# Optimization experiments

Hardware: AMD Instinct MI355X
Metric: run time of the kernel (lower is better)

Reference implementation:

```python
import jax, jax.numpy as jnp
import numpy as np

H = 4096        # hidden_size
NH = 32         # num query heads
NKV = 8         # num kv heads
D = H // NH     # head_dim = 128
S = 2048        # num tokens (single causal sequence)
THETA = 1000000.0
SCALE = D ** -0.5


def _rope(x, positions):
    # neox-style (rotate-half) RoPE over full head_dim, as vLLM's get_rope default
    half = D // 2
    inv_freq = 1.0 / (THETA ** (jnp.arange(half, dtype=jnp.float32) / half))
    ang = positions.astype(jnp.float32)[:, None] * inv_freq          # [S, D/2]
    cos = jnp.cos(ang)[:, None, :]                                   # [S, 1, D/2]
    sin = jnp.sin(ang)[:, None, :]
    x1, x2 = x[..., :half], x[..., half:]
    return jnp.concatenate([x1 * cos - x2 * sin, x2 * cos + x1 * sin], axis=-1)


def setup_inputs() -> dict:
    key = jax.random.key(0)
    k1, k2, k3 = jax.random.split(key, 3)
    positions = jnp.arange(S, dtype=jnp.int32)
    hidden_states = jax.random.normal(k1, (S, H), dtype=jnp.float32)
    w_qkv = jax.random.normal(k2, ((NH + 2 * NKV) * D, H), dtype=jnp.float32) * 0.02
    w_o = jax.random.normal(k3, (H, NH * D), dtype=jnp.float32) * 0.02
    return {"positions": positions, "hidden_states": hidden_states,
            "w_qkv": w_qkv, "w_o": w_o}


def reference(positions, hidden_states, w_qkv, w_o):
    # fused QKV projection (Linear, bias=False): x @ W^T
    qkv = hidden_states @ w_qkv.T                                    # [S, (NH+2*NKV)*D]
    q, k, v = jnp.split(qkv, [NH * D, (NH + NKV) * D], axis=-1)
    q = q.reshape(S, NH, D)
    k = k.reshape(S, NKV, D)
    v = v.reshape(S, NKV, D)
    # RoPE on q and k
    q = _rope(q, positions)
    k = _rope(k, positions)
    # GQA causal attention: group NH query heads onto NKV kv heads
    g = NH // NKV
    qg = q.reshape(S, NKV, g, D)
    scores = jnp.einsum('qhgd,khd->hgqk', qg, k) * SCALE             # [NKV, g, S, S]
    causal = positions[:, None] >= positions[None, :]                # [S, S]
    scores = jnp.where(causal[None, None], scores, jnp.float32(-1e30))
    probs = jax.nn.softmax(scores, axis=-1)
    o = jnp.einsum('hgqk,khd->qhgd', probs, v).reshape(S, NH * D)
    return o @ w_o.T                                                 # [S, H]
```

## Files before the change

### kernel.cpp

```cpp
#include <hip/hip_runtime.h>
#include <hip/hip_bf16.h>

#define S_LEN 2048
#define HID 4096
#define NH 32
#define NKV 8
#define DH 128
#define QKV_N ((NH + 2 * NKV) * DH)
#define SCALE_ATT 0.08838834764831845f
#define SCALE2_ATT 0.12751744f

typedef __bf16 bf16;
typedef __bf16 bf16x8 __attribute__((ext_vector_type(8)));
typedef __bf16 bf16x4 __attribute__((ext_vector_type(4)));
typedef float f32x4 __attribute__((ext_vector_type(4)));
typedef float f32x16 __attribute__((ext_vector_type(16)));

__device__ inline f32x4 mfma16(bf16x8 a, bf16x8 b, f32x4 c) {
    return __builtin_amdgcn_mfma_f32_16x16x32_bf16(a, b, c, 0, 0, 0);
}
__device__ inline f32x16 mfma32(bf16x8 a, bf16x8 b, f32x16 c) {
    return __builtin_amdgcn_mfma_f32_32x32x16_bf16(a, b, c, 0, 0, 0);
}

__device__ inline bf16x8 load8(const float* p) {
    const float4 a = ((const float4*)p)[0];
    const float4 b = ((const float4*)p)[1];
    bf16x8 r;
    r[0] = (bf16)a.x; r[1] = (bf16)a.y; r[2] = (bf16)a.z; r[3] = (bf16)a.w;
    r[4] = (bf16)b.x; r[5] = (bf16)b.y; r[6] = (bf16)b.z; r[7] = (bf16)b.w;
    return r;
}
__device__ inline bf16x8 load8(const bf16* p) { return *(const bf16x8*)p; }

__device__ inline void load_lds16(const bf16* g, bf16* lds_base) {
    __builtin_amdgcn_global_load_lds(
        (const __attribute__((address_space(1))) void*)g,
        (__attribute__((address_space(3))) void*)lds_base, 16, 0, 0);
}

__device__ inline unsigned pack2_bf16(float lo, float hi) {
    union { bf16 h[2]; unsigned u; } r;
    r.h[0] = (bf16)lo;
    r.h[1] = (bf16)hi;
    return r.u;
}

__global__ __launch_bounds__(256) void cvt3_kernel(const float* __restrict__ s0, bf16* __restrict__ d0, int c0,
                                                   const float* __restrict__ s1, bf16* __restrict__ d1, int c1,
                                                   const float* __restrict__ s2, bf16* __restrict__ d2, int c2) {
    int i = blockIdx.x * 256 + threadIdx.x;
    if (i < c0) { *(bf16x8*)&d0[(size_t)i * 8] = load8(&s0[(size_t)i * 8]); return; }
    i -= c0;
    if (i < c1) { *(bf16x8*)&d1[(size_t)i * 8] = load8(&s1[(size_t)i * 8]); return; }
    i -= c1;
    if (i < c2) { *(bf16x8*)&d2[(size_t)i * 8] = load8(&s2[(size_t)i * 8]); }
}

template <int BN, typename OutT>
__global__ __launch_bounds__(512, 2) void gemm_8ph(const bf16* __restrict__ A,
                                                   const bf16* __restrict__ B,
                                                   OutT* __restrict__ C,
                                                   int K, int lda, int ldc) {
    constexpr int WTN = BN / 4;
    constexpr int NREP = WTN / 32;
    constexpr int BLOADS = BN / 64;
    extern __shared__ char smem[];
    bf16* As = (bf16*)smem;
    bf16* Bs = (bf16*)(smem + 2 * 256 * 64 * 2);

    const int tid = threadIdx.x;
    const int lane = tid & 63;
    const int w = tid >> 6;
    const int wm = w >> 2;
    const int wn = w & 3;
    const int ln = lane & 31;
    const int hi = lane >> 5;
    const int rseg = lane >> 3;
    const int gc = (lane & 7) ^ rseg;

    const int m0 = (int)blockIdx.y * 256;
    const int n0 = (int)blockIdx.x * BN;

    const int NT = K >> 6;

    auto stage = [&](int b, int kt) {
        const int k0 = kt * 64;
        const bf16* Ag = &A[(size_t)(m0 + w * 32 + rseg) * lda + k0 + gc * 8];
        bf16* Al = &As[b * (256 * 64) + (w * 32) * 64];
#pragma unroll
        for (int j = 0; j < 4; ++j)
            load_lds16(Ag + (size_t)j * 8 * lda, Al + j * 512);
        const bf16* Bg = &B[(size_t)(n0 + w * (BN / 8) + rseg) * K + k0 + gc * 8];
        bf16* Bl = &Bs[b * (BN * 64) + (w * (BN / 8)) * 64];
#pragma unroll
        for (int j = 0; j < BLOADS; ++j)
            load_lds16(Bg + (size_t)j * 8 * K, Bl + j * 512);
    };

    f32x16 acc[4][NREP];
#pragma unroll
    for (int mi = 0; mi < 4; ++mi)
#pragma unroll
        for (int j = 0; j < NREP; ++j)
#pragma unroll
            for (int r = 0; r < 16; ++r) acc[mi][j][r] = 0.f;

    stage(0, 0);
    int buf = 0;
    for (int kt = 0; kt < NT; ++kt) {
        if (kt + 1 < NT) {
            stage(buf ^ 1, kt + 1);
            if constexpr (BN == 256)
                asm volatile("s_waitcnt vmcnt(8)" ::: "memory");
            else
                asm volatile("s_waitcnt vmcnt(6)" ::: "memory");
        } else {
            asm volatile("s_waitcnt vmcnt(0)" ::: "memory");
        }
        __builtin_amdgcn_s_barrier();
        __builtin_amdgcn_sched_barrier(0);

        const bf16* Ab = &As[buf * (256 * 64)];
        const bf16* Bb = &Bs[buf * (BN * 64)];
        bf16x8 bfr[NREP][4];
#pragma unroll
        for (int j = 0; j < NREP; ++j)
#pragma unroll
            for (int kk = 0; kk < 4; ++kk) {
                const int n = wn * WTN + j * 32 + ln;
                bfr[j][kk] = *(const bf16x8*)&Bb[n * 64 + (((2 * kk + hi) ^ (ln & 7)) * 8)];
            }
#pragma unroll
        for (int p = 0; p < 2; ++p) {
            bf16x8 af[2][4];
#pragma unroll
            for (int i = 0; i < 2; ++i)
#pragma unroll
                for (int kk = 0; kk < 4; ++kk) {
                    const int m = wm * 128 + (p * 2 + i) * 32 + ln;
                    af[i][kk] = *(const bf16x8*)&Ab[m * 64 + (((2 * kk + hi) ^ (ln & 7)) * 8)];
                }
            __builtin_amdgcn_s_setprio(1);
#pragma unroll
            for (int i = 0; i < 2; ++i)
#pragma unroll
                for (int j = 0; j < NREP; ++j)
#pragma unroll
                    for (int kk = 0; kk < 4; ++kk)
                        acc[p * 2 + i][j] = mfma32(af[i][kk], bfr[j][kk], acc[p * 2 + i][j]);
            __builtin_amdgcn_s_setprio(0);
        }
        __builtin_amdgcn_sched_barrier(0);
        asm volatile("s_waitcnt lgkmcnt(0)" ::: "memory");
        __builtin_amdgcn_s_barrier();
        __builtin_amdgcn_sched_barrier(0);
        buf ^= 1;
    }

#pragma unroll
    for (int mi = 0; mi < 4; ++mi)
#pragma unroll
        for (int j = 0; j < NREP; ++j)
#pragma unroll
            for (int r = 0; r < 16; ++r) {
                int row = m0 + wm * 128 + mi * 32 + (r & 3) + 8 * (r >> 2) + 4 * hi;
                int col = n0 + wn * WTN + j * 32 + ln;
                C[(size_t)row * ldc + col] = (OutT)acc[mi][j][r];
            }
}

template <typename AT, typename OutT>
__global__ __launch_bounds__(256) void gemm_bt(const AT* __restrict__ A,
                                               const float* __restrict__ B,
                                               OutT* __restrict__ C,
                                               int K, int lda, int ldc) {
    const int tid = threadIdx.x;
    const int lane = tid & 63;
    const int w = tid >> 6;
    const int m0 = blockIdx.y * 128;
    const int n0 = blockIdx.x * 128;
    const int wm = (w >> 1) * 64;
    const int wn = (w & 1) * 64;
    const int ln = lane & 15;
    const int qo = lane >> 4;

    __shared__ bf16 As[128 * 72];
    __shared__ bf16 Bs[128 * 72];

    f32x4 acc[4][4];
#pragma unroll
    for (int mi = 0; mi < 4; ++mi)
#pragma unroll
        for (int ni = 0; ni < 4; ++ni) acc[mi][ni] = f32x4{0.f, 0.f, 0.f, 0.f};

    for (int k0 = 0; k0 < K; k0 += 64) {
#pragma unroll
        for (int i = 0; i < 4; ++i) {
            int v = tid + i * 256;
            int row = v >> 3;
            int col = (v & 7) * 8;
            *(bf16x8*)&As[row * 72 + col] = load8(&A[(size_t)(m0 + row) * lda + k0 + col]);
            *(bf16x8*)&Bs[row * 72 + col] = load8(&B[(size_t)(n0 + row) * K + k0 + col]);
        }
        __syncthreads();
#pragma unroll
        for (int kk = 0; kk < 64; kk += 32) {
            bf16x8 af[4], bfr[4];
#pragma unroll
            for (int mi = 0; mi < 4; ++mi)
                af[mi] = *(const bf16x8*)&As[(wm + mi * 16 + ln) * 72 + kk + qo * 8];
#pragma unroll
            for (int ni = 0; ni < 4; ++ni)
                bfr[ni] = *(const bf16x8*)&Bs[(wn + ni * 16 + ln) * 72 + kk + qo * 8];
#pragma unroll
            for (int mi = 0; mi < 4; ++mi)
#pragma unroll
                for (int ni = 0; ni < 4; ++ni)
                    acc[mi][ni] = mfma16(af[mi], bfr[ni], acc[mi][ni]);
        }
        __syncthreads();
    }
#pragma unroll
    for (int mi = 0; mi < 4; ++mi)
#pragma unroll
        for (int ni = 0; ni < 4; ++ni)
#pragma unroll
            for (int r = 0; r < 4; ++r) {
                int row = m0 + wm + mi * 16 + qo * 4 + r;
                int col = n0 + wn + ni * 16 + ln;
                C[(size_t)row * ldc + col] = (OutT)acc[mi][ni][r];
            }
}

__global__ __launch_bounds__(256) void rope_kernel(bf16* __restrict__ qkv,
                                                   const int* __restrict__ positions) {
    int idx = blockIdx.x * 256 + threadIdx.x;
    const int total = S_LEN * (NH + NKV) * 64;
    if (idx >= total) return;
    int d = idx & 63;
    int t = idx >> 6;
    int head = t % (NH + NKV);
    int s = t / (NH + NKV);
    size_t base = (size_t)s * QKV_N + (head < NH ? head * DH : NH * DH + (head - NH) * DH);
    float x1 = (float)qkv[base + d];
    float x2 = (float)qkv[base + d + 64];
    float pos = (float)positions[s];
    float inv = expf(-0.21586735246819178f * (float)d);
    float ang = pos * inv;
    float c = cosf(ang);
    float sn = sinf(ang);
    qkv[base + d] = (bf16)(x1 * c - x2 * sn);
    qkv[base + d + 64] = (bf16)(x2 * c + x1 * sn);
}

__global__ __launch_bounds__(256) void vtrans_kernel(const bf16* __restrict__ qkv,
                                                     bf16* __restrict__ vt_g) {
    const int tid = threadIdx.x;
    const int s0 = blockIdx.x * 64;
    const int kvh = blockIdx.y;
    __shared__ bf16 Ls[64 * 136];
#pragma unroll
    for (int i = 0; i < 4; ++i) {
        int v = tid + i * 256;
        int row = v >> 4;
        int col = (v & 15) * 8;
        *(bf16x8*)&Ls[row * 136 + col] =
            *(const bf16x8*)&qkv[(size_t)(s0 + row) * QKV_N + (NH + NKV) * DH + kvh * DH + col];
    }
    __syncthreads();
#pragma unroll
    for (int i = 0; i < 4; ++i) {
        int u = tid + i * 256;
        int d = u >> 3;
        int sg = (u & 7) * 8;
        bf16x8 r;
#pragma unroll
        for (int j = 0; j < 8; ++j) r[j] = Ls[(sg + j) * 136 + d];
        *(bf16x8*)&vt_g[((size_t)kvh * DH + d) * S_LEN + s0 + sg] = r;
    }
}

__global__ __launch_bounds__(256) void attn_kernel(bf16* __restrict__ qkv,
                                                   const bf16* __restrict__ vt_g) {
    const int tid = threadIdx.x;
    const int lane = tid & 63;
    const int w = tid >> 6;
    const int ln = lane & 31;
    const int hi = lane >> 5;
    const int hq = blockIdx.x;
    const int qtile = (int)gridDim.y - 1 - (int)blockIdx.y;
    const int kvh = hq >> 2;
    const int q0 = qtile * 128;
    const int qrow = q0 + w * 32 + ln;

    __shared__ __align__(128) bf16 Ks[2][64 * 128];
    __shared__ __align__(128) bf16 Vt[2][128 * 64];

    bf16x8 qf[8];
    {
        const bf16* qptr = qkv + (size_t)qrow * QKV_N + hq * DH + hi * 8;
#pragma unroll
        for (int s = 0; s < 8; ++s) qf[s] = *(const bf16x8*)(qptr + s * 16);
    }

    const bf16* ksrc = qkv + NH * DH + kvh * DH;
    const bf16* vsrc = vt_g + (size_t)kvh * DH * S_LEN;
    const int kcK = lane & 15;
    const int krs = lane >> 4;
    const int kcV = lane & 7;
    const int vrs = lane >> 3;

    auto stage = [&](int buf, int kt) {
        const int k0s = kt * 64;
#pragma unroll
        for (int j = 0; j < 4; ++j) {
            int r = w * 16 + j * 4 + krs;
            load_lds16(ksrc + (size_t)(k0s + r) * QKV_N + ((kcK ^ (r & 7)) * 8),
                       &Ks[buf][(w * 16 + j * 4) * 128]);
        }
#pragma unroll
        for (int j = 0; j < 4; ++j) {
            int d = w * 32 + j * 8 + vrs;
            load_lds16(vsrc + (size_t)d * S_LEN + k0s + ((kcV ^ (d & 7)) * 8),
                       &Vt[buf][(w * 32 + j * 8) * 64]);
        }
    };

    f32x16 acc[4];
#pragma unroll
    for (int t = 0; t < 4; ++t)
#pragma unroll
        for (int r = 0; r < 16; ++r) acc[t][r] = 0.f;
    float m2 = -1e30f, l = 0.f;

    const int kt_last = (q0 + 127) >> 6;
    int buf = 0;
    stage(0, 0);
    __syncthreads();

    for (int kt = 0; kt <= kt_last; ++kt) {
        if (kt < kt_last) stage(buf ^ 1, kt + 1);
        const int k0 = kt * 64;
        if (k0 <= q0 + w * 32 + 31) {
            f32x16 st[2];
#pragma unroll
            for (int t = 0; t < 2; ++t)
#pragma unroll
                for (int r = 0; r < 16; ++r) st[t][r] = 0.f;
            const bf16* Kb = &Ks[buf][0];
            __builtin_amdgcn_s_setprio(1);
#pragma unroll
            for (int t = 0; t < 2; ++t) {
                const int key = t * 32 + ln;
#pragma unroll
                for (int s = 0; s < 8; ++s) {
                    bf16x8 kf =
                        *(const bf16x8*)&Kb[key * 128 + (((2 * s + hi) ^ (key & 7)) * 8)];
                    st[t] = mfma32(kf, qf[s], st[t]);
                }
            }
            __builtin_amdgcn_s_setprio(0);
            const bool needMask = (k0 + 63 > q0 + w * 32);
            float tmax = -1e30f;
#pragma unroll
            for (int t = 0; t < 2; ++t)
#pragma unroll
                for (int r = 0; r < 16; ++r) {
                    int kcol = k0 + t * 32 + (r & 3) + 8 * (r >> 2) + 4 * hi;
                    float v = st[t][r] * SCALE2_ATT;
                    if (needMask && kcol > qrow) v = -1e30f;
                    st[t][r] = v;
                    tmax = fmaxf(tmax, v);
                }
            tmax = fmaxf(tmax, __shfl_xor(tmax, 32, 64));
            float mnew = fmaxf(m2, tmax);
            float alpha = exp2f(m2 - mnew);
            float rs = 0.f;
#pragma unroll
            for (int t = 0; t < 2; ++t)
#pragma unroll
                for (int r = 0; r < 16; ++r) {
                    float e = exp2f(st[t][r] - mnew);
                    st[t][r] = e;
                    rs += e;
                }
            rs += __shfl_xor(rs, 32, 64);
            l = l * alpha + rs;
            m2 = mnew;
#pragma unroll
            for (int t = 0; t < 4; ++t)
#pragma unroll
                for (int r = 0; r < 16; ++r) acc[t][r] *= alpha;
            unsigned cw[16];
#pragma unroll
            for (int i = 0; i < 16; ++i)
                cw[i] = pack2_bf16(st[i >> 3][2 * (i & 7)], st[i >> 3][2 * (i & 7) + 1]);
            bf16x8 pa[4];
#pragma unroll
            for (int ks = 0; ks < 4; ++ks) {
                const int base = (ks >> 1) * 8 + (ks & 1) * 4;
                union { unsigned u[4]; bf16x8 v; } pk;
#pragma unroll
                for (int e = 0; e < 2; ++e) {
                    unsigned A = cw[base + e];
                    unsigned B = cw[base + 2 + e];
                    unsigned tA = (unsigned)__shfl_xor((int)A, 32, 64);
                    unsigned tB = (unsigned)__shfl_xor((int)B, 32, 64);
                    pk.u[e] = hi ? tB : A;
                    pk.u[e + 2] = hi ? B : tA;
                }
                pa[ks] = pk.v;
            }
            const bf16* Vb = &Vt[buf][0];
            __builtin_amdgcn_s_setprio(1);
#pragma unroll
            for (int dt = 0; dt < 4; ++dt) {
                const int d = dt * 32 + ln;
#pragma unroll
                for (int ks = 0; ks < 4; ++ks) {
                    bf16x8 vf =
                        *(const bf16x8*)&Vb[d * 64 + (((2 * ks + hi) ^ (d & 7)) * 8)];
                    acc[dt] = mfma32(vf, pa[ks], acc[dt]);
                }
            }
            __builtin_amdgcn_s_setprio(0);
        }
        __syncthreads();
        buf ^= 1;
    }

    const float invl = 1.f / l;
    bf16* outp = qkv + (size_t)qrow * QKV_N + hq * DH;
#pragma unroll
    for (int dt = 0; dt < 4; ++dt)
#pragma unroll
        for (int rq = 0; rq < 4; ++rq) {
            bf16x4 o;
#pragma unroll
            for (int i = 0; i < 4; ++i) o[i] = (bf16)(acc[dt][rq * 4 + i] * invl);
            *(bf16x4*)(outp + dt * 32 + rq * 8 + hi * 4) = o;
        }
}

extern "C" void kernel_launch(void* const* d_in, const int* in_sizes, int n_in,
                              void* d_out, int out_size, void* d_ws, size_t ws_size,
                              hipStream_t stream) {
    const int* positions = (const int*)d_in[0];
    const float* hidden = (const float*)d_in[1];
    const float* w_qkv = (const float*)d_in[2];
    const float* w_o = (const float*)d_in[3];
    float* out = (float*)d_out;

    const size_t n_qkv = (size_t)S_LEN * QKV_N;
    const size_t n_vt = (size_t)NKV * DH * S_LEN;
    const size_t n_hid = (size_t)S_LEN * HID;
    const size_t n_wqkv = (size_t)QKV_N * HID;
    const size_t n_wo = (size_t)HID * HID;

    const size_t need_min = (n_qkv + n_vt) * sizeof(bf16);
    const size_t need_full = (n_qkv + n_vt + n_hid + n_wqkv + n_wo) * sizeof(bf16);
    if (ws_size < need_min) return;

    bf16* qkv = (bf16*)d_ws;
    bf16* vt_g = qkv + n_qkv;
    bf16* hid_b = vt_g + n_vt;
    bf16* wqkv_b = hid_b + n_hid;
    bf16* wo_b = wqkv_b + n_wqkv;
    const bool full = ws_size >= need_full;

    if (full) {
        const int c0 = (int)(n_hid / 8), c1 = (int)(n_wqkv / 8), c2 = (int)(n_wo / 8);
        cvt3_kernel<<<(c0 + c1 + c2 + 255) / 256, 256, 0, stream>>>(hidden, hid_b, c0,
                                                                    w_qkv, wqkv_b, c1,
                                                                    w_o, wo_b, c2);
        hipFuncSetAttribute(reinterpret_cast<const void*>(&gemm_8ph<256, bf16>),
                            hipFuncAttributeMaxDynamicSharedMemorySize, 131072);
        gemm_8ph<256, bf16><<<dim3(QKV_N / 256, S_LEN / 256), 512, 131072, stream>>>(
            hid_b, wqkv_b, qkv, HID, HID, QKV_N);
    } else {
        gemm_bt<<<dim3(QKV_N / 128, S_LEN / 128), 256, 0, stream>>>(hidden, w_qkv, qkv, HID, HID, QKV_N);
    }
    const int total = S_LEN * (NH + NKV) * 64;
    rope_kernel<<<(total + 255) / 256, 256, 0, stream>>>(qkv, positions);
    vtrans_kernel<<<dim3(S_LEN / 64, NKV), 256, 0, stream>>>(qkv, vt_g);
    attn_kernel<<<dim3(NH, S_LEN / 128), 256, 0, stream>>>(qkv, vt_g);
    if (full) {
        hipFuncSetAttribute(reinterpret_cast<const void*>(&gemm_8ph<128, float>),
                            hipFuncAttributeMaxDynamicSharedMemorySize, 98304);
        gemm_8ph<128, float><<<dim3(HID / 128, S_LEN / 256), 512, 98304, stream>>>(
            qkv, wo_b, out, HID, QKV_N, HID);
    } else {
        gemm_bt<<<dim3(HID / 128, S_LEN / 128), 256, 0, stream>>>(qkv, w_o, out, HID, QKV_N, HID);
    }
}
```

Baseline: 572.6 us.

## Interleave global-to-LDS prefetch with MFMA phases in gemm_8ph main loop

Restructures the GEMM main loop into four sub-phases per K-tile, each issuing a slice of the next tiles' global-to-LDS loads (A one tile ahead, B two tiles ahead into the just-consumed buffer) between fragment reads and MFMAs. The goal is to spread memory traffic evenly across compute and avoid the bursty stage-then-wait pattern. It adds more barriers per iteration and tighter vmcnt bookkeeping, which carries a risk of stalls or a subtle race if the counts are off.

```diff
diff --git a/kernel.cpp b/kernel.cpp
--- a/kernel.cpp
+++ b/kernel.cpp
@@ -64,7 +64,6 @@
                                                    int K, int lda, int ldc) {
     constexpr int WTN = BN / 4;
     constexpr int NREP = WTN / 32;
-    constexpr int BLOADS = BN / 64;
     extern __shared__ char smem[];
     bf16* As = (bf16*)smem;
     bf16* Bs = (bf16*)(smem + 2 * 256 * 64 * 2);
@@ -81,22 +80,31 @@
 
     const int m0 = (int)blockIdx.y * 256;
     const int n0 = (int)blockIdx.x * BN;
-
     const int NT = K >> 6;
 
-    auto stage = [&](int b, int kt) {
+    auto stageA = [&](int pb, int kt, int h) {
         const int k0 = kt * 64;
-        const bf16* Ag = &A[(size_t)(m0 + w * 32 + rseg) * lda + k0 + gc * 8];
-        bf16* Al = &As[b * (256 * 64) + (w * 32) * 64];
-#pragma unroll
-        for (int j = 0; j < 4; ++j)
-            load_lds16(Ag + (size_t)j * 8 * lda, Al + j * 512);
-        const bf16* Bg = &B[(size_t)(n0 + w * (BN / 8) + rseg) * K + k0 + gc * 8];
-        bf16* Bl = &Bs[b * (BN * 64) + (w * (BN / 8)) * 64];
-#pragma unroll
-        for (int j = 0; j < BLOADS; ++j)
-            load_lds16(Bg + (size_t)j * 8 * K, Bl + j * 512);
+        const int rb = h * 128 + w * 16;
+        const bf16* src = &A[(size_t)(m0 + rb + rseg) * lda + k0 + gc * 8];
+        bf16* dst = &As[pb * (256 * 64) + rb * 64];
+        load_lds16(src, dst);
+        load_lds16(src + (size_t)8 * lda, dst + 8 * 64);
     };
+    auto stageB = [&](int pb, int kt, int h) {
+        const int k0 = kt * 64;
+        if constexpr (BN == 256) {
+            const int rb = h * 128 + w * 16;
+            const bf16* src = &B[(size_t)(n0 + rb + rseg) * K + k0 + gc * 8];
+            bf16* dst = &Bs[pb * (BN * 64) + rb * 64];
+            load_lds16(src, dst);
+            load_lds16(src + (size_t)8 * K, dst + 8 * 64);
+        } else {
+            const int rb = h * 64 + w * 8;
+            const bf16* src = &B[(size_t)(n0 + rb + rseg) * K + k0 + gc * 8];
+            bf16* dst = &Bs[pb * (BN * 64) + rb * 64];
+            load_lds16(src, dst);
+        }
+    };
 
     f32x16 acc[4][NREP];
 #pragma unroll
@@ -106,57 +114,68 @@
 #pragma unroll
             for (int r = 0; r < 16; ++r) acc[mi][j][r] = 0.f;
 
-    stage(0, 0);
-    int buf = 0;
-    for (int kt = 0; kt < NT; ++kt) {
-        if (kt + 1 < NT) {
-            stage(buf ^ 1, kt + 1);
-            if constexpr (BN == 256)
-                asm volatile("s_waitcnt vmcnt(8)" ::: "memory");
-            else
-                asm volatile("s_waitcnt vmcnt(6)" ::: "memory");
-        } else {
-            asm volatile("s_waitcnt vmcnt(0)" ::: "memory");
-        }
-        __builtin_amdgcn_s_barrier();
-        __builtin_amdgcn_sched_barrier(0);
-
-        const bf16* Ab = &As[buf * (256 * 64)];
-        const bf16* Bb = &Bs[buf * (BN * 64)];
+    stageB(0, 0, 0); stageB(0, 0, 1);
+    stageA(0, 0, 0); stageA(0, 0, 1);
+    {
+        const int k1 = NT > 1 ? 1 : 0;
+        stageB(1, k1, 0); stageB(1, k1, 1);
+    }
+    if constexpr (BN == 256)
+        asm volatile("s_waitcnt vmcnt(4)" ::: "memory");
+    else
+        asm volatile("s_waitcnt vmcnt(2)" ::: "memory");
+    __builtin_amdgcn_s_barrier();
+
+    int p = 0;
+    for (int u = 0; u < NT; ++u, p ^= 1) {
+        const bf16* Ab = &As[p * (256 * 64)];
+        const bf16* Bb = &Bs[p * (BN * 64)];
+        const int ktA = u + 1 < NT ? u + 1 : NT - 1;
+        const int ktB = u + 2 < NT ? u + 2 : NT - 1;
         bf16x8 bfr[NREP][4];
 #pragma unroll
-        for (int j = 0; j < NREP; ++j)
+        for (int q = 0; q < 4; ++q) {
+            if (q == 0) {
+#pragma unroll
+                for (int j = 0; j < NREP; ++j)
+#pragma unroll
+                    for (int kk = 0; kk < 4; ++kk) {
+                        const int n = wn * WTN + j * 32 + ln;
+                        bfr[j][kk] = *(const bf16x8*)&Bb[n * 64 + (((2 * kk + hi) ^ (ln & 7)) * 8)];
+                    }
+            }
+            bf16x8 af[4];
 #pragma unroll
             for (int kk = 0; kk < 4; ++kk) {
-                const int n = wn * WTN + j * 32 + ln;
-                bfr[j][kk] = *(const bf16x8*)&Bb[n * 64 + (((2 * kk + hi) ^ (ln & 7)) * 8)];
-            }
-#pragma unroll
-        for (int p = 0; p < 2; ++p) {
-            bf16x8 af[2][4];
-#pragma unroll
-            for (int i = 0; i < 2; ++i)
-#pragma unroll
-                for (int kk = 0; kk < 4; ++kk) {
-                    const int m = wm * 128 + (p * 2 + i) * 32 + ln;
-                    af[i][kk] = *(const bf16x8*)&Ab[m * 64 + (((2 * kk + hi) ^ (ln & 7)) * 8)];
-                }
+                const int m = wm * 128 + q * 32 + ln;
+                af[kk] = *(const bf16x8*)&Ab[m * 64 + (((2 * kk + hi) ^ (ln & 7)) * 8)];
+            }
+            if (q == 0) stageA(p ^ 1, ktA, 0);
+            else if (q == 1) stageA(p ^ 1, ktA, 1);
+            else if (q == 2) stageB(p, ktB, 0);
+            else stageB(p, ktB, 1);
+
+            __builtin_amdgcn_s_barrier();
+            asm volatile("s_waitcnt lgkmcnt(0)" ::: "memory");
+            __builtin_amdgcn_sched_barrier(0);
             __builtin_amdgcn_s_setprio(1);
 #pragma unroll
-            for (int i = 0; i < 2; ++i)
-#pragma unroll
-                for (int j = 0; j < NREP; ++j)
-#pragma unroll
-                    for (int kk = 0; kk < 4; ++kk)
-                        acc[p * 2 + i][j] = mfma32(af[i][kk], bfr[j][kk], acc[p * 2 + i][j]);
+            for (int j = 0; j < NREP; ++j)
+#pragma unroll
+                for (int kk = 0; kk < 4; ++kk)
+                    acc[q][j] = mfma32(af[kk], bfr[j][kk], acc[q][j]);
             __builtin_amdgcn_s_setprio(0);
-        }
-        __builtin_amdgcn_sched_barrier(0);
-        asm volatile("s_waitcnt lgkmcnt(0)" ::: "memory");
-        __builtin_amdgcn_s_barrier();
-        __builtin_amdgcn_sched_barrier(0);
-        buf ^= 1;
-    }
+            __builtin_amdgcn_sched_barrier(0);
+            if (q == 3) {
+                if constexpr (BN == 256)
+                    asm volatile("s_waitcnt vmcnt(4)" ::: "memory");
+                else
+                    asm volatile("s_waitcnt vmcnt(2)" ::: "memory");
+            }
+            __builtin_amdgcn_s_barrier();
+        }
+    }
+    asm volatile("s_waitcnt vmcnt(0)" ::: "memory");
 
 #pragma unroll
     for (int mi = 0; mi < 4; ++mi)
```

Result: faster. 537.2 us (-6.2%).
